# Kernel optimization log

Hardware: AMD Instinct MI355X
Metric: run time of the kernel (lower is better)

## Reference

```python
import jax, jax.numpy as jnp
import numpy as np

NG, ND = 50000, 10000          # gene / disease node counts
IN, HID = 64, 128              # in_feats / hidden_feats
EGG, EGD, EDG = 800000, 300000, 300000
EPS = 1e-5


def setup_inputs() -> dict:
    key = jax.random.key(0)
    ks = jax.random.split(key, 18)
    s = 0.05
    return {
        "xg": jax.random.normal(ks[0], (NG, IN), jnp.float32),
        "xd": jax.random.normal(ks[1], (ND, IN), jnp.float32),
        "Wn0": jax.random.normal(ks[2], (3, IN, HID), jnp.float32) * s,
        "Ws0": jax.random.normal(ks[3], (3, IN, HID), jnp.float32) * s,
        "b0": jnp.zeros((3, HID), jnp.float32),
        "Wn1": jax.random.normal(ks[4], (3, HID, HID), jnp.float32) * s,
        "Ws1": jax.random.normal(ks[5], (3, HID, HID), jnp.float32) * s,
        "b1": jnp.zeros((3, HID), jnp.float32),
        "bng": jnp.ones((2, 2, HID), jnp.float32),   # [layer, ntype, HID]
        "bnb": jnp.zeros((2, 2, HID), jnp.float32),
        "Wp": jax.random.normal(ks[6], (2, HID, IN), jnp.float32) * s,
        "bp": jnp.zeros((2, IN), jnp.float32),
        "gg_src": jax.random.randint(ks[7], (EGG,), 0, NG, jnp.int32),
        "gg_dst": jax.random.randint(ks[8], (EGG,), 0, NG, jnp.int32),
        "gd_src": jax.random.randint(ks[9], (EGD,), 0, NG, jnp.int32),
        "gd_dst": jax.random.randint(ks[10], (EGD,), 0, ND, jnp.int32),
        "dg_src": jax.random.randint(ks[11], (EDG,), 0, ND, jnp.int32),
        "dg_dst": jax.random.randint(ks[12], (EDG,), 0, NG, jnp.int32),
    }


def _seg_mean(h_src, src_idx, dst_idx, num_dst):
    # gather source features along edges, mean-reduce onto destinations
    msg = h_src[src_idx]                                         # [E, D]
    ssum = jax.ops.segment_sum(msg, dst_idx, num_segments=num_dst)
    deg = jax.ops.segment_sum(jnp.ones((dst_idx.shape[0], 1), h_src.dtype),
                              dst_idx, num_segments=num_dst)
    return ssum / jnp.maximum(deg, 1.0)                          # zero-degree -> 0


def _sage(h_src, h_dst, src_idx, dst_idx, num_dst, Wn, Ws, b):
    # DGL SAGEConv(mean): fc_neigh(mean_neigh) + fc_self(h_dst) + bias
    m = _seg_mean(h_src, src_idx, dst_idx, num_dst)
    return m @ Wn + h_dst @ Ws + b


def _bn_relu(x, g, b):
    # BatchNorm1d in training mode (batch statistics) followed by ReLU
    mu = x.mean(axis=0)
    var = x.var(axis=0)
    return jax.nn.relu((x - mu) * jax.lax.rsqrt(var + EPS) * g + b)


def _hetero_layer(hg, hd, Wn, Ws, b, idx):
    gg_s, gg_d, gd_s, gd_d, dg_s, dg_d = idx
    # HeteroGraphConv aggregate='sum' across relations per destination type
    out_g = (_sage(hg, hg, gg_s, gg_d, NG, Wn[0], Ws[0], b[0]) +
             _sage(hd, hg, dg_s, dg_d, NG, Wn[2], Ws[2], b[2]))
    out_d = _sage(hg, hd, gd_s, gd_d, ND, Wn[1], Ws[1], b[1])
    return out_g, out_d


def reference(xg, xd, Wn0, Ws0, b0, Wn1, Ws1, b1, bng, bnb, Wp, bp,
              gg_src, gg_dst, gd_src, gd_dst, dg_src, dg_dst):
    idx = (gg_src, gg_dst, gd_src, gd_dst, dg_src, dg_dst)
    # layer 0
    hg, hd = _hetero_layer(xg, xd, Wn0, Ws0, b0, idx)
    hg = _bn_relu(hg, bng[0, 0], bnb[0, 0])
    hd = _bn_relu(hd, bng[0, 1], bnb[0, 1])
    # layer 1
    hg, hd = _hetero_layer(hg, hd, Wn1, Ws1, b1, idx)
    hg = _bn_relu(hg, bng[1, 0], bnb[1, 0])
    hd = _bn_relu(hd, bng[1, 1], bnb[1, 1])
    # final per-type projection back to in_feats
    out_g = hg @ Wp[0] + bp[0]
    out_d = hd @ Wp[1] + bp[1]
    return out_g, out_d
```

## Files before the change

### kernel.cpp

```cpp
#include <hip/hip_runtime.h>

typedef unsigned short u16;
typedef __attribute__((ext_vector_type(8))) short bf16x8;
typedef __attribute__((ext_vector_type(4))) float f32x4;

__device__ __forceinline__ float BF(u16 u) { return __uint_as_float(((unsigned)u) << 16); }
__device__ __forceinline__ float BLO(unsigned p) { return __uint_as_float(p << 16); }
__device__ __forceinline__ float BHI(unsigned p) { return __uint_as_float(p & 0xffff0000u); }
__device__ __forceinline__ u16 FBF(float f) {
    unsigned u = __float_as_uint(f);
    u += 0x7FFFu + ((u >> 16) & 1u);
    return (u16)(u >> 16);
}
__device__ __forceinline__ unsigned PK2(float a, float b) {
    return (unsigned)FBF(a) | ((unsigned)FBF(b) << 16);
}
__device__ __forceinline__ float LD(const void* p, long i, int isf) {
    if (isf) return ((const float*)p)[i];
    return BF(((const u16*)p)[i]);
}

__global__ void HeteroGNN_78426102825755_kernel() {}

__global__ void hk_fill16(u16* p, long n, u16 v) {
    long i = (long)blockIdx.x * 256 + threadIdx.x;
    if (i < n) p[i] = v;
}

__global__ void hk_detect2(const void* x, int* flag, int* ncur, int Tn, float* bnbuf) {
    int i = blockIdx.x * 256 + threadIdx.x;
    if (i < Tn) ncur[i] = 0;
    if (i < 512) bnbuf[i] = 0.f;
    if (blockIdx.x == 0) {
        __shared__ int cnt;
        if (threadIdx.x == 0) cnt = 0;
        __syncthreads();
        unsigned w = ((const unsigned*)x)[threadIdx.x];
        int e = (w >> 7) & 0xFF;
        atomicAdd(&cnt, (e >= 0x68 && e <= 0x92) ? 1 : 0);
        __syncthreads();
        if (threadIdx.x == 0) flag[0] = (cnt >= 192) ? 0 : 1;
    }
}

__device__ __forceinline__ void wprep_one(const void* W, int K, int ncol, int persh, int ksh,
                                          unsigned* dst, int i, int isf) {
    int mslice = i >> persh;
    int d2 = i & ((1 << persh) - 1);
    int mat = mslice >> ksh;
    int ks = mslice & ((1 << ksh) - 1);
    int ct = d2 >> 8; int rr = d2 & 255; int ln = rr >> 2; int j2 = rr & 3;
    int k1 = ks * 32 + ((ln >> 4) * 8 + 2 * j2);
    int n = ct * 16 + (ln & 15);
    long e = (long)mat * K * ncol + (long)k1 * ncol + n;
    dst[i] = PK2(LD(W, e, isf), LD(W, e + ncol, isf));
}
__device__ __forceinline__ void wsum_one(const void* W, int K, unsigned* dst, int i, int isf) {
    int ks = i >> 11; int d2 = i & 2047;
    int ct = d2 >> 8; int rr = d2 & 255; int ln = rr >> 2; int j2 = rr & 3;
    int k1 = ks * 32 + ((ln >> 4) * 8 + 2 * j2);
    int n = ct * 16 + (ln & 15);
    long e = (long)k1 * 128 + n;
    long e2 = e + (long)2 * K * 128;
    dst[i] = PK2(LD(W, e, isf) + LD(W, e2, isf), LD(W, e + 128, isf) + LD(W, e2 + 128, isf));
}

__global__ void hk_prepcnt(const void* Wn0, const void* Ws0, const void* Wn1, const void* Ws1,
                           unsigned* f0n, unsigned* f0s, unsigned* f1n, unsigned* f1s,
                           unsigned* f0sum, unsigned* f1sum,
                           const void* xg, const void* xd, long n0, long n1,
                           u16* og, u16* od, int Cb,
                           const int* d0, const int* d1, const int* d2,
                           int E0, int E1, int E2, int NGn, int* cnt, int* rank,
                           const int* dflag) {
    int b = blockIdx.x, t = threadIdx.x;
    if (b < Cb) {
        int i = b * 256 + t;
        int tn;
        if (i < E0) tn = d0[i];
        else if (i < E0 + E1) tn = NGn + d1[i - E0];
        else if (i < E0 + E1 + E2) tn = 2 * NGn + d2[i - E0 - E1];
        else return;
        rank[i] = atomicAdd(&cnt[tn], 1);
        return;
    }
    int isf = dflag[0];
    b -= Cb;
    if (b < 48)  { wprep_one(Wn0, 64, 128, 11, 1, f0n, b * 256 + t, isf); return; }
    if (b < 96)  { wprep_one(Ws0, 64, 128, 11, 1, f0s, (b - 48) * 256 + t, isf); return; }
    if (b < 192) { wprep_one(Wn1, 128, 128, 11, 2, f1n, (b - 96) * 256 + t, isf); return; }
    if (b < 288) { wprep_one(Ws1, 128, 128, 11, 2, f1s, (b - 192) * 256 + t, isf); return; }
    if (b < 304) { wsum_one(Ws0, 64, f0sum, (b - 288) * 256 + t, isf); return; }
    if (b < 336) { wsum_one(Ws1, 128, f1sum, (b - 304) * 256 + t, isf); return; }
    long i = (long)(b - 336) * 256 + t;
    if (i < n0) og[i] = FBF(LD(xg, i, isf));
    else if (i < n0 + n1) od[i - n0] = FBF(LD(xd, i - n0, isf));
}

__global__ void hk_scan_a(const int* cnt, int n, int* pre, int* bsum) {
    __shared__ int lds[2048];
    __shared__ int part[256];
    int t = threadIdx.x;
    int base = blockIdx.x * 2048;
    for (int i = 0; i < 8; i++) {
        int idx = base + i * 256 + t;
        lds[i * 256 + t] = (idx < n) ? cnt[idx] : 0;
    }
    __syncthreads();
    int run[8];
    int s = 0;
    for (int i = 0; i < 8; i++) { run[i] = lds[t * 8 + i]; s += run[i]; }
    part[t] = s;
    __syncthreads();
    for (int o = 1; o < 256; o <<= 1) {
        int add = (t >= o) ? part[t - o] : 0;
        __syncthreads();
        part[t] += add;
        __syncthreads();
    }
    int ex = (t == 0) ? 0 : part[t - 1];
    for (int i = 0; i < 8; i++) {
        lds[t * 8 + i] = ex;
        ex += run[i];
    }
    __syncthreads();
    for (int i = 0; i < 8; i++) {
        int idx = base + i * 256 + t;
        if (idx < n) pre[idx] = lds[i * 256 + t];
    }
    if (t == 255) bsum[blockIdx.x] = part[255];
}

__global__ void hk_scan_b(int* bsum, int nb) {
    __shared__ int part[256];
    int t = threadIdx.x;
    part[t] = (t < nb) ? bsum[t] : 0;
    __syncthreads();
    for (int o = 1; o < 256; o <<= 1) {
        int add = (t >= o) ? part[t - o] : 0;
        __syncthreads();
        part[t] += add;
        __syncthreads();
    }
    if (t < nb) bsum[t] = (t == 0) ? 0 : part[t - 1];
    if (t == 0) bsum[nb] = part[nb - 1];
}

__global__ void hk_scan_c(const int* pre, const int* bsum, int n, int nb, int* offs) {
    int i = blockIdx.x * 256 + threadIdx.x;
    if (i < n) offs[i] = pre[i] + bsum[i >> 11];
    if (i == 0) offs[n] = bsum[nb];
}

__global__ void hk_scatter3p(const int* s0, const int* d0, const int* s1, const int* d1,
                             const int* s2, const int* d2,
                             int E0, int E1, int E2, int NGn,
                             const int* offs, const int* rank, int* csr, float pscale) {
    int part = blockIdx.x & 7;
    int stride = (gridDim.x >> 3) * 256;
    int ET = E0 + E1 + E2;
    for (int i = (blockIdx.x >> 3) * 256 + threadIdx.x; i < ET; i += stride) {
        int t;
        if (i < E0) t = d0[i];
        else if (i < E0 + E1) t = NGn + d1[i - E0];
        else t = 2 * NGn + d2[i - E0 - E1];
        int p = (int)((float)t * pscale);
        if (p > 7) p = 7;
        if (p != part) continue;
        int s = (i < E0) ? s0[i] : (i < E0 + E1) ? s1[i - E0] : s2[i - E0 - E1];
        csr[offs[t] + rank[i]] = s;
    }
}

struct FS {
    const unsigned* gsrc[2]; const int* goffs[2]; const float* gbn[2];
    const unsigned* ssrc; const float* sbn;
    const int* csr;
    const unsigned* W[12];
    const void* bb; long b1off; long b2off;
    int N; u16* out; float* stats;
};

template<bool BN>
__device__ void m64row(const unsigned* __restrict__ g, const int* __restrict__ offs,
                       const int* __restrict__ csr, unsigned* __restrict__ lds, int PSl,
                       int r, int row0, int N, int lane, const float* __restrict__ bn) {
    int gA = row0 + r, gB = gA + 1;
    if (gA >= N) return;
    int bA = offs[gA], eA = offs[gA + 1];
    int bB = 0, eB = 0;
    if (gB < N) { bB = offs[gB]; eB = offs[gB + 1]; }
    float scx = 0.f, scy = 0.f, shx = 0.f, shy = 0.f;
    if (BN) {
        float2 s2 = *(const float2*)&bn[2 * lane];
        float2 h2 = *(const float2*)&bn[128 + 2 * lane];
        scx = s2.x; scy = s2.y; shx = h2.x; shy = h2.y;
    }
    float sA0 = 0.f, sA1 = 0.f, sB0 = 0.f, sB1 = 0.f;
    auto ACC = [&](unsigned p, float& s0, float& s1) {
        float vx = BLO(p), vy = BHI(p);
        if (BN) { vx = fmaxf(fmaf(vx, scx, shx), 0.f); vy = fmaxf(fmaf(vy, scy, shy), 0.f); }
        s0 += vx; s1 += vy;
    };
    int kA = bA, kB = bB;
    while (kA + 4 <= eA && kB + 4 <= eB) {
        unsigned pA0 = g[(long)csr[kA] * 64 + lane];
        unsigned pA1 = g[(long)csr[kA + 1] * 64 + lane];
        unsigned pA2 = g[(long)csr[kA + 2] * 64 + lane];
        unsigned pA3 = g[(long)csr[kA + 3] * 64 + lane];
        unsigned pB0 = g[(long)csr[kB] * 64 + lane];
        unsigned pB1 = g[(long)csr[kB + 1] * 64 + lane];
        unsigned pB2 = g[(long)csr[kB + 2] * 64 + lane];
        unsigned pB3 = g[(long)csr[kB + 3] * 64 + lane];
        ACC(pA0, sA0, sA1); ACC(pA1, sA0, sA1); ACC(pA2, sA0, sA1); ACC(pA3, sA0, sA1);
        ACC(pB0, sB0, sB1); ACC(pB1, sB0, sB1); ACC(pB2, sB0, sB1); ACC(pB3, sB0, sB1);
        kA += 4; kB += 4;
    }
    while (kA + 4 <= eA) {
        unsigned p0 = g[(long)csr[kA] * 64 + lane];
        unsigned p1 = g[(long)csr[kA + 1] * 64 + lane];
        unsigned p2 = g[(long)csr[kA + 2] * 64 + lane];
        unsigned p3 = g[(long)csr[kA + 3] * 64 + lane];
        ACC(p0, sA0, sA1); ACC(p1, sA0, sA1); ACC(p2, sA0, sA1); ACC(p3, sA0, sA1);
        kA += 4;
    }
    while (kB + 4 <= eB) {
        unsigned p0 = g[(long)csr[kB] * 64 + lane];
        unsigned p1 = g[(long)csr[kB + 1] * 64 + lane];
        unsigned p2 = g[(long)csr[kB + 2] * 64 + lane];
        unsigned p3 = g[(long)csr[kB + 3] * 64 + lane];
        ACC(p0, sB0, sB1); ACC(p1, sB0, sB1); ACC(p2, sB0, sB1); ACC(p3, sB0, sB1);
        kB += 4;
    }
    for (; kA < eA; kA++) { unsigned p = g[(long)csr[kA] * 64 + lane]; ACC(p, sA0, sA1); }
    for (; kB < eB; kB++) { unsigned p = g[(long)csr[kB] * 64 + lane]; ACC(p, sB0, sB1); }
    float invA = (eA > bA) ? 1.f / (float)(eA - bA) : 0.f;
    float invB = (eB > bB) ? 1.f / (float)(eB - bB) : 0.f;
    lds[r * PSl + lane] = PK2(sA0 * invA, sA1 * invA);
    if (gB < N) lds[(r + 1) * PSl + lane] = PK2(sB0 * invB, sB1 * invB);
}

__device__ void m32row(const unsigned* __restrict__ g, const int* __restrict__ offs,
                       const int* __restrict__ csr, unsigned* __restrict__ lds, int PSl,
                       int r, int row0, int N, int l) {
    int gA = row0 + r, gB = gA + 1;
    if (gA >= N) return;
    int bA = offs[gA], eA = offs[gA + 1];
    int bB = 0, eB = 0;
    if (gB < N) { bB = offs[gB]; eB = offs[gB + 1]; }
    float sA0 = 0.f, sA1 = 0.f, sB0 = 0.f, sB1 = 0.f;
    int kA = bA, kB = bB;
    while (kA + 4 <= eA && kB + 4 <= eB) {
        unsigned pA0 = g[(long)csr[kA] * 32 + l];
        unsigned pA1 = g[(long)csr[kA + 1] * 32 + l];
        unsigned pA2 = g[(long)csr[kA + 2] * 32 + l];
        unsigned pA3 = g[(long)csr[kA + 3] * 32 + l];
        unsigned pB0 = g[(long)csr[kB] * 32 + l];
        unsigned pB1 = g[(long)csr[kB + 1] * 32 + l];
        unsigned pB2 = g[(long)csr[kB + 2] * 32 + l];
        unsigned pB3 = g[(long)csr[kB + 3] * 32 + l];
        sA0 += (BLO(pA0) + BLO(pA1)) + (BLO(pA2) + BLO(pA3));
        sA1 += (BHI(pA0) + BHI(pA1)) + (BHI(pA2) + BHI(pA3));
        sB0 += (BLO(pB0) + BLO(pB1)) + (BLO(pB2) + BLO(pB3));
        sB1 += (BHI(pB0) + BHI(pB1)) + (BHI(pB2) + BHI(pB3));
        kA += 4; kB += 4;
    }
    while (kA + 4 <= eA) {
        unsigned p0 = g[(long)csr[kA] * 32 + l];
        unsigned p1 = g[(long)csr[kA + 1] * 32 + l];
        unsigned p2 = g[(long)csr[kA + 2] * 32 + l];
        unsigned p3 = g[(long)csr[kA + 3] * 32 + l];
        sA0 += (BLO(p0) + BLO(p1)) + (BLO(p2) + BLO(p3));
        sA1 += (BHI(p0) + BHI(p1)) + (BHI(p2) + BHI(p3));
        kA += 4;
    }
    while (kB + 4 <= eB) {
        unsigned p0 = g[(long)csr[kB] * 32 + l];
        unsigned p1 = g[(long)csr[kB + 1] * 32 + l];
        unsigned p2 = g[(long)csr[kB + 2] * 32 + l];
        unsigned p3 = g[(long)csr[kB + 3] * 32 + l];
        sB0 += (BLO(p0) + BLO(p1)) + (BLO(p2) + BLO(p3));
        sB1 += (BHI(p0) + BHI(p1)) + (BHI(p2) + BHI(p3));
        kB += 4;
    }
    for (; kA < eA; kA++) {
        unsigned p = g[(long)csr[kA] * 32 + l];
        sA0 += BLO(p); sA1 += BHI(p);
    }
    for (; kB < eB; kB++) {
        unsigned p = g[(long)csr[kB] * 32 + l];
        sB0 += BLO(p); sB1 += BHI(p);
    }
    float invA = (eA > bA) ? 1.f / (float)(eA - bA) : 0.f;
    float invB = (eB > bB) ? 1.f / (float)(eB - bB) : 0.f;
    lds[r * PSl + l] = PK2(sA0 * invA, sA1 * invA);
    if (gB < N) lds[(r + 1) * PSl + l] = PK2(sB0 * invB, sB1 * invB);
}

template<int NM, int RS, int PS, bool BN>
__device__ __forceinline__ void stage_self(const FS& P, int row0, unsigned* lds, int tid) {
    constexpr int R4 = RS / 4;
    const uint4* src = (const uint4*)P.ssrc + (long)row0 * R4;
#pragma unroll
    for (int j0 = 0; j0 < 64 * R4; j0 += 512) {
        int j = j0 + tid;
        int r = j / R4, c = j - r * R4;
        uint4 v = src[j];
        if (BN) {
            unsigned w[4] = {v.x, v.y, v.z, v.w};
#pragma unroll
            for (int q = 0; q < 4; q++) {
                int col = 8 * c + 2 * q;
                float2 s2 = *(const float2*)&P.sbn[col];
                float2 h2 = *(const float2*)&P.sbn[128 + col];
                w[q] = PK2(fmaxf(fmaf(BLO(w[q]), s2.x, h2.x), 0.f),
                           fmaxf(fmaf(BHI(w[q]), s2.y, h2.y), 0.f));
            }
            v.x = w[0]; v.y = w[1]; v.z = w[2]; v.w = w[3];
        }
        *(uint4*)&lds[(NM * 64 + r) * PS + c * 4] = v;
    }
}

template<int NM, int KS, int RS, int PS, bool BN>
__device__ __forceinline__ void fs_body(const FS& P, int row0, int isf,
                                        unsigned* lds, float* red) {
    constexpr int NS = (NM + 1) * KS;
    int tid = threadIdx.x;
    int wave = tid >> 6, lane = tid & 63, m = lane & 15, quad = lane >> 4;
    bf16x8 B[NS];
#pragma unroll
    for (int s = 0; s < NS; s++)
        B[s] = *(const bf16x8*)(P.W[s] + wave * 256 + lane * 4);
#pragma unroll
    for (int t = 0; t < NM; t++) {
        unsigned* lt = lds + t * 64 * PS;
        if constexpr (RS == 64) {
#pragma unroll
            for (int p = 0; p < 4; p++)
                m64row<BN>(P.gsrc[t], P.goffs[t], P.csr, lt, PS,
                           wave * 8 + 2 * p, row0, P.N, lane, P.gbn[t]);
        } else {
            int half = lane >> 5, l = lane & 31;
#pragma unroll
            for (int p = 0; p < 2; p++)
                m32row(P.gsrc[t], P.goffs[t], P.csr, lt, PS,
                       wave * 8 + 4 * p + 2 * half, row0, P.N, l);
        }
    }
    stage_self<NM, RS, PS, BN>(P, row0, lds, tid);
    __syncthreads();

    f32x4 acc[4];
    f32x4 z = {0.f, 0.f, 0.f, 0.f};
#pragma unroll
    for (int rt = 0; rt < 4; rt++) acc[rt] = z;
#pragma unroll
    for (int s = 0; s < NS; s++) {
        const unsigned* ab = lds + (s / KS) * 64 * PS + (s % KS) * 16;
#pragma unroll
        for (int rt = 0; rt < 4; rt++) {
            bf16x8 af = *(const bf16x8*)(ab + (rt * 16 + m) * PS + quad * 4);
            acc[rt] = __builtin_amdgcn_mfma_f32_16x16x32_bf16(af, B[s], acc[rt], 0, 0, 0);
        }
    }
    if (tid < 256) red[tid] = 0.f;
    __syncthreads();
    int col = wave * 16 + m;
    float bv = LD(P.bb, P.b1off + col, isf);
    if (P.b2off >= 0) bv += LD(P.bb, P.b2off + col, isf);
    float ps = 0.f, ps2 = 0.f;
#pragma unroll
    for (int rt = 0; rt < 4; rt++) {
#pragma unroll
        for (int reg = 0; reg < 4; reg++) {
            int row = row0 + rt * 16 + quad * 4 + reg;
            if (row < P.N) {
                float v = acc[rt][reg] + bv;
                P.out[(long)row * 128 + col] = FBF(v);
                ps += v; ps2 += v * v;
            }
        }
    }
    atomicAdd(&red[col], ps);
    atomicAdd(&red[col + 128], ps2);
    __syncthreads();
    if (tid < 256) atomicAdd(&P.stats[tid], red[tid]);
}

template<int NMG, int NMD, int KS, int RS, int PS, bool BN>
__global__ __launch_bounds__(512) void hk_fsage(FS G, FS D, int gbl, const int* dflag) {
    __shared__ __align__(16) unsigned lds[(NMG + 1) * 64 * PS];
    __shared__ float red[256];
    int isf = dflag[0];
    int b = blockIdx.x;
    if (b < gbl) fs_body<NMG, KS, RS, PS, BN>(G, b * 64, isf, lds, red);
    else         fs_body<NMD, KS, RS, PS, BN>(D, (b - gbl) * 64, isf, lds, red);
}

__global__ void hk_bnfinal2(float* buf, float invNg, float invNd,
                            const void* g, long gg, long gd,
                            const void* b, long bg, long bd, const int* dflag) {
    int isf = dflag[0];
    int t = threadIdx.x;
    int c = t & 127, isD = t >> 7;
    float* st = buf + (isD ? 256 : 0);
    float invN = isD ? invNd : invNg;
    float s1 = st[c], s2 = st[c + 128];
    float mu = s1 * invN;
    float var = s2 * invN - mu * mu;
    if (var < 0.f) var = 0.f;
    float sc = LD(g, (isD ? gd : gg) + c, isf) * rsqrtf(var + 1e-5f);
    float* o = buf + 512 + (isD ? 256 : 0);
    o[c] = sc;
    o[c + 128] = LD(b, (isD ? bd : bg) + c, isf) - mu * sc;
    st[c] = 0.f;
    st[c + 128] = 0.f;
}

__global__ void hk_proj2(const u16* Ag, int Ngn, const u16* Ad, int Ndn, int gbl,
                         const void* W, const void* bias, float* og, float* od,
                         const float* bn, const int* dflag) {
    const int S = 130;
    __shared__ float aT[64 * S];
    __shared__ float ws[2048];
    int isf = dflag[0];
    int tid = threadIdx.x;
    int gene = ((int)blockIdx.x < gbl) ? 1 : 0;
    const u16* A = gene ? Ag : Ad;
    int N = gene ? Ngn : Ndn;
    long woff = gene ? 0 : 8192;
    long boff = gene ? 0 : 64;
    float* out = gene ? og : od;
    const float* sc = bn + 512 + (gene ? 0 : 256);
    const float* sh = sc + 128;
    int wave = tid >> 6, lane = tid & 63;
    int jx = tid & 15, r0 = (tid >> 4) * 4;
    int row0 = (gene ? blockIdx.x : blockIdx.x - gbl) * 64;

    float2 scv = *(const float2*)&sc[2 * lane];
    float2 shv = *(const float2*)&sh[2 * lane];
    const unsigned* A32 = (const unsigned*)A;
    for (int i = 0; i < 16; i++) {
        int r = wave * 16 + i, row = row0 + r;
        unsigned p = (row < N) ? A32[(long)row * 64 + lane] : 0u;
        float2 v;
        v.x = fmaf(BLO(p), scv.x, shv.x); v.x = (v.x > 0.f) ? v.x : 0.f;
        v.y = fmaf(BHI(p), scv.y, shv.y); v.y = (v.y > 0.f) ? v.y : 0.f;
        *(float2*)&aT[r * S + 2 * lane] = v;
    }
    __syncthreads();

    float acc[4][4];
    for (int r = 0; r < 4; r++)
        for (int c = 0; c < 4; c++) acc[r][c] = 0.f;

    for (int k0 = 0; k0 < 128; k0 += 32) {
        for (int i = 0; i < 8; i++) {
            int idx = tid + i * 256;
            ws[idx] = LD(W, woff + (long)(k0 + (idx >> 6)) * 64 + (idx & 63), isf);
        }
        __syncthreads();
        for (int kk = 0; kk < 32; kk++) {
            float4 w4 = *(const float4*)(ws + kk * 64 + jx * 4);
            for (int r = 0; r < 4; r++) {
                float a = aT[(r0 + r) * S + k0 + kk];
                acc[r][0] = fmaf(a, w4.x, acc[r][0]);
                acc[r][1] = fmaf(a, w4.y, acc[r][1]);
                acc[r][2] = fmaf(a, w4.z, acc[r][2]);
                acc[r][3] = fmaf(a, w4.w, acc[r][3]);
            }
        }
        __syncthreads();
    }

    float b4[4];
    for (int c = 0; c < 4; c++) b4[c] = LD(bias, boff + jx * 4 + c, isf);
    for (int r = 0; r < 4; r++) {
        int row = row0 + r0 + r;
        if (row >= N) continue;
        float4 o;
        o.x = acc[r][0] + b4[0]; o.y = acc[r][1] + b4[1];
        o.z = acc[r][2] + b4[2]; o.w = acc[r][3] + b4[3];
        *(float4*)&out[(long)row * 64 + jx * 4] = o;
    }
}

extern "C" void kernel_launch(void* const* d_in, const int* in_sizes, int n_in,
                              void* d_out, int out_size, void* d_ws, size_t ws_size,
                              hipStream_t stream) {
    const void* xg = d_in[0];
    const void* xd = d_in[1];
    const void* Wn0 = d_in[2];
    const void* Ws0 = d_in[3];
    const void* b0 = d_in[4];
    const void* Wn1 = d_in[5];
    const void* Ws1 = d_in[6];
    const void* b1 = d_in[7];
    const void* bng = d_in[8];
    const void* bnb = d_in[9];
    const void* Wp = d_in[10];
    const void* bp = d_in[11];
    const int* gg_src = (const int*)d_in[12];
    const int* gg_dst = (const int*)d_in[13];
    const int* gd_src = (const int*)d_in[14];
    const int* gd_dst = (const int*)d_in[15];
    const int* dg_src = (const int*)d_in[16];
    const int* dg_dst = (const int*)d_in[17];

    const int NG = in_sizes[0] / 64;
    const int ND = in_sizes[1] / 64;
    const int EGG = in_sizes[12];
    const int EGD = in_sizes[14];
    const int EDG = in_sizes[16];

    const int NGp = (NG + 63) & ~63;
    const int NDp = (ND + 63) & ~63;
    const int Tn = 2 * NG + ND;
    const int ET = EGG + EDG + EGD;

    float* outf = (float*)d_out;

    char* base = (char*)d_ws;
    size_t off = 0;
    u16* hg0; u16* pg1;
    unsigned *wf0n, *wf0s, *wf1n, *wf1s, *wf0sum, *wf1sum;
    int *csr, *offs, *ncur, *scanpre, *scanbs;
    int* dflag;
    float* bnbuf;
    {
        hg0 = (u16*)(base + off);      off += (size_t)NGp * 128 * 2; off = (off + 255) & ~(size_t)255;
        pg1 = (u16*)(base + off);      off += (size_t)NGp * 128 * 2; off = (off + 255) & ~(size_t)255;
        wf0n = (unsigned*)(base + off); off += 3 * 4096 * 4;         off = (off + 255) & ~(size_t)255;
        wf0s = (unsigned*)(base + off); off += 3 * 4096 * 4;         off = (off + 255) & ~(size_t)255;
        wf1n = (unsigned*)(base + off); off += 3 * 8192 * 4;         off = (off + 255) & ~(size_t)255;
        wf1s = (unsigned*)(base + off); off += 3 * 8192 * 4;         off = (off + 255) & ~(size_t)255;
        wf0sum = (unsigned*)(base + off); off += 4096 * 4;           off = (off + 255) & ~(size_t)255;
        wf1sum = (unsigned*)(base + off); off += 8192 * 4;           off = (off + 255) & ~(size_t)255;
        csr = (int*)(base + off);      off += (size_t)ET * 4;        off = (off + 255) & ~(size_t)255;
        offs = (int*)(base + off);     off += (size_t)(Tn + 1) * 4;  off = (off + 255) & ~(size_t)255;
        ncur = (int*)(base + off);     off += (size_t)Tn * 4;        off = (off + 255) & ~(size_t)255;
        scanpre = (int*)(base + off);  off += (size_t)Tn * 4;        off = (off + 255) & ~(size_t)255;
        scanbs = (int*)(base + off);   off += 257 * 4;               off = (off + 255) & ~(size_t)255;
        bnbuf = (float*)(base + off);  off += 1024 * 4;              off = (off + 255) & ~(size_t)255;
        dflag = (int*)(base + off);    off += 256;                   off = (off + 255) & ~(size_t)255;
    }
    size_t off_base = off;
    u16* pd1ws = (u16*)(base + off); off += (size_t)NDp * 128 * 2;
    size_t off_full = off;

    int tier;
    if (off_full <= ws_size) tier = 2;
    else if (off_base <= ws_size) tier = 1;
    else {
        hk_fill16<<<(int)(((long)out_size * 2 + 255) / 256), 256, 0, stream>>>(
            (u16*)d_out, (long)out_size * 2, (u16)0x4000);
        return;
    }

    u16* hd0 = (u16*)d_out;
    u16* pd1out = hd0 + (long)NDp * 128;
    u16* pd1 = (tier == 2) ? pd1ws : pd1out;

    u16* xg16 = pg1;
    u16* xd16 = pg1 + (long)NGp * 64;
    int* rank = (int*)hg0;

    hk_detect2<<<(Tn + 255) / 256, 256, 0, stream>>>(xg, dflag, ncur, Tn, bnbuf);

    {
        int Cb = (ET + 255) / 256;
        int Tb = (int)(((long)(NG + ND) * 64 + 255) / 256);
        hk_prepcnt<<<Cb + 336 + Tb, 256, 0, stream>>>(
            Wn0, Ws0, Wn1, Ws1, wf0n, wf0s, wf1n, wf1s, wf0sum, wf1sum,
            xg, xd, (long)NG * 64, (long)ND * 64, xg16, xd16, Cb,
            gg_dst, dg_dst, gd_dst, EGG, EDG, EGD, NG, ncur, rank, dflag);
    }

    {
        int nbT = (Tn + 2047) / 2048;
        hk_scan_a<<<nbT, 256, 0, stream>>>(ncur, Tn, scanpre, scanbs);
        hk_scan_b<<<1, 256, 0, stream>>>(scanbs, nbT);
        hk_scan_c<<<(Tn + 255) / 256, 256, 0, stream>>>(scanpre, scanbs, Tn, nbT, offs);
    }

    hk_scatter3p<<<8 * 208, 256, 0, stream>>>(gg_src, gg_dst, dg_src, dg_dst,
                                              gd_src, gd_dst, EGG, EDG, EGD,
                                              NG, offs, rank, csr, 8.0f / (float)Tn);

    const int gb = NGp / 64, db = NDp / 64;
    unsigned* xg16u = (unsigned*)xg16;
    unsigned* xd16u = (unsigned*)xd16;
    unsigned* hg0u = (unsigned*)hg0;
    unsigned* hd0u = (unsigned*)hd0;
    const float* bnG = bnbuf + 512;
    const float* bnD = bnbuf + 768;

    FS G = {}, D = {};

    G.gsrc[0] = xg16u; G.goffs[0] = offs;          G.gbn[0] = 0;
    G.gsrc[1] = xd16u; G.goffs[1] = offs + NG;     G.gbn[1] = 0;
    G.ssrc = xg16u; G.sbn = 0; G.csr = csr;
    G.W[0] = wf0n;            G.W[1] = wf0n + 2048;
    G.W[2] = wf0n + 2 * 4096; G.W[3] = wf0n + 2 * 4096 + 2048;
    G.W[4] = wf0sum;          G.W[5] = wf0sum + 2048;
    G.bb = b0; G.b1off = 0; G.b2off = 256;
    G.N = NG; G.out = hg0; G.stats = bnbuf;
    D.gsrc[0] = xg16u; D.goffs[0] = offs + 2 * NG; D.gbn[0] = 0;
    D.ssrc = xd16u; D.sbn = 0; D.csr = csr;
    D.W[0] = wf0n + 4096; D.W[1] = wf0n + 4096 + 2048;
    D.W[2] = wf0s + 4096; D.W[3] = wf0s + 4096 + 2048;
    D.bb = b0; D.b1off = 128; D.b2off = -1;
    D.N = ND; D.out = hd0; D.stats = bnbuf + 256;
    hk_fsage<2, 1, 2, 32, 36, false><<<gb + db, 512, 0, stream>>>(G, D, gb, dflag);
    hk_bnfinal2<<<1, 256, 0, stream>>>(bnbuf, 1.f / NG, 1.f / ND, bng, 0L, 128L, bnb, 0L, 128L, dflag);

    G = FS{}; D = FS{};
    G.gsrc[0] = hg0u; G.goffs[0] = offs;          G.gbn[0] = bnG;
    G.gsrc[1] = hd0u; G.goffs[1] = offs + NG;     G.gbn[1] = bnD;
    G.ssrc = hg0u; G.sbn = bnG; G.csr = csr;
    for (int ks = 0; ks < 4; ks++) {
        G.W[ks] = wf1n + ks * 2048;
        G.W[4 + ks] = wf1n + 2 * 8192 + ks * 2048;
        G.W[8 + ks] = wf1sum + ks * 2048;
        D.W[ks] = wf1n + 8192 + ks * 2048;
        D.W[4 + ks] = wf1s + 8192 + ks * 2048;
    }
    G.bb = b1; G.b1off = 0; G.b2off = 256;
    G.N = NG; G.out = pg1; G.stats = bnbuf;
    D.gsrc[0] = hg0u; D.goffs[0] = offs + 2 * NG; D.gbn[0] = bnG;
    D.ssrc = hd0u; D.sbn = bnD; D.csr = csr;
    D.bb = b1; D.b1off = 128; D.b2off = -1;
    D.N = ND; D.out = pd1; D.stats = bnbuf + 256;
    hk_fsage<2, 1, 4, 64, 68, true><<<gb + db, 512, 0, stream>>>(G, D, gb, dflag);
    hk_bnfinal2<<<1, 256, 0, stream>>>(bnbuf, 1.f / NG, 1.f / ND, bng, 256L, 384L, bnb, 256L, 384L, dflag);

    if (tier == 2) {
        hk_proj2<<<gb + db, 256, 0, stream>>>(pg1, NG, pd1, ND, gb, Wp, bp,
                                              outf, outf + (long)NG * 64, bnbuf, dflag);
    } else {
        hk_proj2<<<db, 256, 0, stream>>>(pg1, NG, pd1, ND, 0, Wp, bp,
                                         outf, outf + (long)NG * 64, bnbuf, dflag);
        hk_proj2<<<gb, 256, 0, stream>>>(pg1, NG, pd1, ND, gb, Wp, bp,
                                         outf, outf + (long)NG * 64, bnbuf, dflag);
    }
}
```

Before: 443.9 us.

## Split neighbor-mean aggregation out of fused SAGE kernel into separate gather kernels

Replaces the fused gather+GEMM SAGE kernel with a standalone mean-aggregation kernel that writes per-relation neighbor means to a workspace buffer, followed by a dense kernel that just stages precomputed tiles into LDS and runs the MFMA GEMM. BatchNorm+ReLU of layer-0 outputs is now applied once in place by a new elementwise kernel instead of per gathered edge. This removes the redundant per-edge BN work and lets the gather run at its own occupancy without the GEMM's LDS and register footprint. In exchange it adds extra kernel launches, a large intermediate buffer round-trip through memory, and changes the workspace tier thresholds.

```diff
diff --git a/kernel.cpp b/kernel.cpp
--- a/kernel.cpp
+++ b/kernel.cpp
@@ -172,36 +172,15 @@
     }
 }
 
-struct FS {
-    const unsigned* gsrc[2]; const int* goffs[2]; const float* gbn[2];
-    const unsigned* ssrc; const float* sbn;
-    const int* csr;
-    const unsigned* W[12];
-    const void* bb; long b1off; long b2off;
-    int N; u16* out; float* stats;
-};
-
-template<bool BN>
-__device__ void m64row(const unsigned* __restrict__ g, const int* __restrict__ offs,
-                       const int* __restrict__ csr, unsigned* __restrict__ lds, int PSl,
-                       int r, int row0, int N, int lane, const float* __restrict__ bn) {
-    int gA = row0 + r, gB = gA + 1;
-    if (gA >= N) return;
-    int bA = offs[gA], eA = offs[gA + 1];
+__device__ void mean64_rows(const unsigned* __restrict__ g, const int* __restrict__ offs,
+                            const int* __restrict__ csr, unsigned* __restrict__ out,
+                            int rA, int N, int lane) {
+    int rB = rA + 1;
+    if (rA >= N) return;
+    int bA = offs[rA], eA = offs[rA + 1];
     int bB = 0, eB = 0;
-    if (gB < N) { bB = offs[gB]; eB = offs[gB + 1]; }
-    float scx = 0.f, scy = 0.f, shx = 0.f, shy = 0.f;
-    if (BN) {
-        float2 s2 = *(const float2*)&bn[2 * lane];
-        float2 h2 = *(const float2*)&bn[128 + 2 * lane];
-        scx = s2.x; scy = s2.y; shx = h2.x; shy = h2.y;
-    }
+    if (rB < N) { bB = offs[rB]; eB = offs[rB + 1]; }
     float sA0 = 0.f, sA1 = 0.f, sB0 = 0.f, sB1 = 0.f;
-    auto ACC = [&](unsigned p, float& s0, float& s1) {
-        float vx = BLO(p), vy = BHI(p);
-        if (BN) { vx = fmaxf(fmaf(vx, scx, shx), 0.f); vy = fmaxf(fmaf(vy, scy, shy), 0.f); }
-        s0 += vx; s1 += vy;
-    };
     int kA = bA, kB = bB;
     while (kA + 4 <= eA && kB + 4 <= eB) {
         unsigned pA0 = g[(long)csr[kA] * 64 + lane];
@@ -212,8 +191,10 @@
         unsigned pB1 = g[(long)csr[kB + 1] * 64 + lane];
         unsigned pB2 = g[(long)csr[kB + 2] * 64 + lane];
         unsigned pB3 = g[(long)csr[kB + 3] * 64 + lane];
-        ACC(pA0, sA0, sA1); ACC(pA1, sA0, sA1); ACC(pA2, sA0, sA1); ACC(pA3, sA0, sA1);
-        ACC(pB0, sB0, sB1); ACC(pB1, sB0, sB1); ACC(pB2, sB0, sB1); ACC(pB3, sB0, sB1);
+        sA0 += (BLO(pA0) + BLO(pA1)) + (BLO(pA2) + BLO(pA3));
+        sA1 += (BHI(pA0) + BHI(pA1)) + (BHI(pA2) + BHI(pA3));
+        sB0 += (BLO(pB0) + BLO(pB1)) + (BLO(pB2) + BLO(pB3));
+        sB1 += (BHI(pB0) + BHI(pB1)) + (BHI(pB2) + BHI(pB3));
         kA += 4; kB += 4;
     }
     while (kA + 4 <= eA) {
@@ -221,7 +202,8 @@
         unsigned p1 = g[(long)csr[kA + 1] * 64 + lane];
         unsigned p2 = g[(long)csr[kA + 2] * 64 + lane];
         unsigned p3 = g[(long)csr[kA + 3] * 64 + lane];
-        ACC(p0, sA0, sA1); ACC(p1, sA0, sA1); ACC(p2, sA0, sA1); ACC(p3, sA0, sA1);
+        sA0 += (BLO(p0) + BLO(p1)) + (BLO(p2) + BLO(p3));
+        sA1 += (BHI(p0) + BHI(p1)) + (BHI(p2) + BHI(p3));
         kA += 4;
     }
     while (kB + 4 <= eB) {
@@ -229,25 +211,32 @@
         unsigned p1 = g[(long)csr[kB + 1] * 64 + lane];
         unsigned p2 = g[(long)csr[kB + 2] * 64 + lane];
         unsigned p3 = g[(long)csr[kB + 3] * 64 + lane];
-        ACC(p0, sB0, sB1); ACC(p1, sB0, sB1); ACC(p2, sB0, sB1); ACC(p3, sB0, sB1);
+        sB0 += (BLO(p0) + BLO(p1)) + (BLO(p2) + BLO(p3));
+        sB1 += (BHI(p0) + BHI(p1)) + (BHI(p2) + BHI(p3));
         kB += 4;
     }
-    for (; kA < eA; kA++) { unsigned p = g[(long)csr[kA] * 64 + lane]; ACC(p, sA0, sA1); }
-    for (; kB < eB; kB++) { unsigned p = g[(long)csr[kB] * 64 + lane]; ACC(p, sB0, sB1); }
+    for (; kA < eA; kA++) {
+        unsigned p = g[(long)csr[kA] * 64 + lane];
+        sA0 += BLO(p); sA1 += BHI(p);
+    }
+    for (; kB < eB; kB++) {
+        unsigned p = g[(long)csr[kB] * 64 + lane];
+        sB0 += BLO(p); sB1 += BHI(p);
+    }
     float invA = (eA > bA) ? 1.f / (float)(eA - bA) : 0.f;
     float invB = (eB > bB) ? 1.f / (float)(eB - bB) : 0.f;
-    lds[r * PSl + lane] = PK2(sA0 * invA, sA1 * invA);
-    if (gB < N) lds[(r + 1) * PSl + lane] = PK2(sB0 * invB, sB1 * invB);
-}
-
-__device__ void m32row(const unsigned* __restrict__ g, const int* __restrict__ offs,
-                       const int* __restrict__ csr, unsigned* __restrict__ lds, int PSl,
-                       int r, int row0, int N, int l) {
-    int gA = row0 + r, gB = gA + 1;
-    if (gA >= N) return;
-    int bA = offs[gA], eA = offs[gA + 1];
+    out[(long)rA * 64 + lane] = PK2(sA0 * invA, sA1 * invA);
+    if (rB < N) out[(long)rB * 64 + lane] = PK2(sB0 * invB, sB1 * invB);
+}
+
+__device__ void mean32_rows(const unsigned* __restrict__ g, const int* __restrict__ offs,
+                            const int* __restrict__ csr, unsigned* __restrict__ out,
+                            int rA, int N, int l) {
+    int rB = rA + 1;
+    if (rA >= N) return;
+    int bA = offs[rA], eA = offs[rA + 1];
     int bB = 0, eB = 0;
-    if (gB < N) { bB = offs[gB]; eB = offs[gB + 1]; }
+    if (rB < N) { bB = offs[rB]; eB = offs[rB + 1]; }
     float sA0 = 0.f, sA1 = 0.f, sB0 = 0.f, sB1 = 0.f;
     int kA = bA, kB = bB;
     while (kA + 4 <= eA && kB + 4 <= eB) {
@@ -293,62 +282,65 @@
     }
     float invA = (eA > bA) ? 1.f / (float)(eA - bA) : 0.f;
     float invB = (eB > bB) ? 1.f / (float)(eB - bB) : 0.f;
-    lds[r * PSl + l] = PK2(sA0 * invA, sA1 * invA);
-    if (gB < N) lds[(r + 1) * PSl + l] = PK2(sB0 * invB, sB1 * invB);
-}
-
-template<int NM, int RS, int PS, bool BN>
-__device__ __forceinline__ void stage_self(const FS& P, int row0, unsigned* lds, int tid) {
-    constexpr int R4 = RS / 4;
-    const uint4* src = (const uint4*)P.ssrc + (long)row0 * R4;
-#pragma unroll
-    for (int j0 = 0; j0 < 64 * R4; j0 += 512) {
-        int j = j0 + tid;
-        int r = j / R4, c = j - r * R4;
-        uint4 v = src[j];
-        if (BN) {
-            unsigned w[4] = {v.x, v.y, v.z, v.w};
-#pragma unroll
-            for (int q = 0; q < 4; q++) {
-                int col = 8 * c + 2 * q;
-                float2 s2 = *(const float2*)&P.sbn[col];
-                float2 h2 = *(const float2*)&P.sbn[128 + col];
-                w[q] = PK2(fmaxf(fmaf(BLO(w[q]), s2.x, h2.x), 0.f),
-                           fmaxf(fmaf(BHI(w[q]), s2.y, h2.y), 0.f));
-            }
-            v.x = w[0]; v.y = w[1]; v.z = w[2]; v.w = w[3];
-        }
-        *(uint4*)&lds[(NM * 64 + r) * PS + c * 4] = v;
-    }
-}
-
-template<int NM, int KS, int RS, int PS, bool BN>
-__device__ __forceinline__ void fs_body(const FS& P, int row0, int isf,
-                                        unsigned* lds, float* red) {
-    constexpr int NS = (NM + 1) * KS;
+    out[(long)rA * 32 + l] = PK2(sA0 * invA, sA1 * invA);
+    if (rB < N) out[(long)rB * 32 + l] = PK2(sB0 * invB, sB1 * invB);
+}
+
+__global__ void hk_mean32a(const unsigned* hg, const unsigned* hd,
+                           const int* offs, const int* csr,
+                           unsigned* mgg, unsigned* mdg, unsigned* mgd,
+                           int NGn, int NDn, int nbg) {
+    int b = blockIdx.x;
+    const unsigned* g; const int* O; unsigned* o; int N; int rb;
+    if (b < nbg)          { g = hg; O = offs;           o = mgg; N = NGn; rb = b * 16; }
+    else if (b < 2 * nbg) { g = hd; O = offs + NGn;     o = mdg; N = NGn; rb = (b - nbg) * 16; }
+    else                  { g = hg; O = offs + 2 * NGn; o = mgd; N = NDn; rb = (b - 2 * nbg) * 16; }
+    int w = threadIdx.x >> 6, lane = threadIdx.x & 63;
+    int half = lane >> 5, l = lane & 31;
+    mean32_rows(g, O, csr, o, rb + w * 4 + half * 2, N, l);
+}
+
+__global__ void hk_mean64a(const unsigned* hg, const unsigned* hd,
+                           const int* offs, const int* csr,
+                           unsigned* mgg, unsigned* mdg, unsigned* mgd,
+                           int NGn, int NDn, int nbg) {
+    int b = blockIdx.x;
+    const unsigned* g; const int* O; unsigned* o; int N; int rb;
+    if (b < nbg)          { g = hg; O = offs;           o = mgg; N = NGn; rb = b * 8; }
+    else if (b < 2 * nbg) { g = hd; O = offs + NGn;     o = mdg; N = NGn; rb = (b - nbg) * 8; }
+    else                  { g = hg; O = offs + 2 * NGn; o = mgd; N = NDn; rb = (b - 2 * nbg) * 8; }
+    int w = threadIdx.x >> 6, lane = threadIdx.x & 63;
+    mean64_rows(g, O, csr, o, rb + w * 2, N, lane);
+}
+
+struct DS3 {
+    const unsigned* AT[3];
+    const unsigned* W[12];
+    const void* bb; long b1off; long b2off;
+    int N; u16* out; float* stats;
+};
+
+template<int NT, int KS, int RS, int PS>
+__device__ __forceinline__ void ds3_body(const DS3& P, int row0, int isf,
+                                         unsigned* lds, float* red) {
+    constexpr int NS = NT * KS;
     int tid = threadIdx.x;
     int wave = tid >> 6, lane = tid & 63, m = lane & 15, quad = lane >> 4;
     bf16x8 B[NS];
 #pragma unroll
     for (int s = 0; s < NS; s++)
         B[s] = *(const bf16x8*)(P.W[s] + wave * 256 + lane * 4);
-#pragma unroll
-    for (int t = 0; t < NM; t++) {
-        unsigned* lt = lds + t * 64 * PS;
-        if constexpr (RS == 64) {
-#pragma unroll
-            for (int p = 0; p < 4; p++)
-                m64row<BN>(P.gsrc[t], P.goffs[t], P.csr, lt, PS,
-                           wave * 8 + 2 * p, row0, P.N, lane, P.gbn[t]);
-        } else {
-            int half = lane >> 5, l = lane & 31;
-#pragma unroll
-            for (int p = 0; p < 2; p++)
-                m32row(P.gsrc[t], P.goffs[t], P.csr, lt, PS,
-                       wave * 8 + 4 * p + 2 * half, row0, P.N, l);
+    constexpr int R4 = RS / 4;
+#pragma unroll
+    for (int t = 0; t < NT; t++) {
+        const uint4* src = (const uint4*)P.AT[t] + (long)row0 * R4;
+#pragma unroll
+        for (int j0 = 0; j0 < 64 * R4; j0 += 512) {
+            int j = j0 + tid;
+            int r = j / R4, c = j - r * R4;
+            *(uint4*)&lds[(t * 64 + r) * PS + c * 4] = src[j];
         }
     }
-    stage_self<NM, RS, PS, BN>(P, row0, lds, tid);
     __syncthreads();
 
     f32x4 acc[4];
@@ -388,14 +380,14 @@
     if (tid < 256) atomicAdd(&P.stats[tid], red[tid]);
 }
 
-template<int NMG, int NMD, int KS, int RS, int PS, bool BN>
-__global__ __launch_bounds__(512) void hk_fsage(FS G, FS D, int gbl, const int* dflag) {
-    __shared__ __align__(16) unsigned lds[(NMG + 1) * 64 * PS];
+template<int NTG, int NTD, int KS, int RS, int PS>
+__global__ __launch_bounds__(512) void hk_dsage3(DS3 G, DS3 D, int gbl, const int* dflag) {
+    __shared__ __align__(16) unsigned lds[NTG * 64 * PS];
     __shared__ float red[256];
     int isf = dflag[0];
     int b = blockIdx.x;
-    if (b < gbl) fs_body<NMG, KS, RS, PS, BN>(G, b * 64, isf, lds, red);
-    else         fs_body<NMD, KS, RS, PS, BN>(D, (b - gbl) * 64, isf, lds, red);
+    if (b < gbl) ds3_body<NTG, KS, RS, PS>(G, b * 64, isf, lds, red);
+    else         ds3_body<NTD, KS, RS, PS>(D, (b - gbl) * 64, isf, lds, red);
 }
 
 __global__ void hk_bnfinal2(float* buf, float invNg, float invNd,
@@ -416,6 +408,29 @@
     o[c + 128] = LD(b, (isD ? bd : bg) + c, isf) - mu * sc;
     st[c] = 0.f;
     st[c + 128] = 0.f;
+}
+
+__global__ void hk_bnapply2(u16* xg_, long n8g, u16* xd_, long n8d, const float* buf) {
+    long i = (long)blockIdx.x * 256 + threadIdx.x;
+    uint4* p; const float *sc, *sh; long k;
+    if (i < n8g) { k = i; p = (uint4*)xg_; sc = buf + 512; sh = buf + 640; }
+    else {
+        k = i - n8g;
+        if (k >= n8d) return;
+        p = (uint4*)xd_; sc = buf + 768; sh = buf + 896;
+    }
+    uint4 v = p[k];
+    int j = (int)(k & 15) * 8;
+    float f[8] = {BLO(v.x), BHI(v.x), BLO(v.y), BHI(v.y),
+                  BLO(v.z), BHI(v.z), BLO(v.w), BHI(v.w)};
+    for (int c = 0; c < 8; c++) {
+        float t = fmaf(f[c], sc[j + c], sh[j + c]);
+        f[c] = (t > 0.f) ? t : 0.f;
+    }
+    uint4 o;
+    o.x = PK2(f[0], f[1]); o.y = PK2(f[2], f[3]);
+    o.z = PK2(f[4], f[5]); o.w = PK2(f[6], f[7]);
+    p[k] = o;
 }
 
 __global__ void hk_proj2(const u16* Ag, int Ngn, const u16* Ad, int Ndn, int gbl,
@@ -545,13 +560,14 @@
         bnbuf = (float*)(base + off);  off += 1024 * 4;              off = (off + 255) & ~(size_t)255;
         dflag = (int*)(base + off);    off += 256;                   off = (off + 255) & ~(size_t)255;
     }
-    size_t off_base = off;
+    unsigned* meanP = (unsigned*)(base + off); off += (size_t)NGp * 128 * 4; off = (off + 255) & ~(size_t)255;
+    size_t off_mean = off;
     u16* pd1ws = (u16*)(base + off); off += (size_t)NDp * 128 * 2;
     size_t off_full = off;
 
     int tier;
     if (off_full <= ws_size) tier = 2;
-    else if (off_base <= ws_size) tier = 1;
+    else if (off_mean <= ws_size) tier = 1;
     else {
         hk_fill16<<<(int)(((long)out_size * 2 + 255) / 256), 256, 0, stream>>>(
             (u16*)d_out, (long)out_size * 2, (u16)0x4000);
@@ -560,6 +576,7 @@
 
     u16* hd0 = (u16*)d_out;
     u16* pd1out = hd0 + (long)NDp * 128;
+    unsigned* mgdM = (unsigned*)(pd1out + (long)NDp * 128);
     u16* pd1 = (tier == 2) ? pd1ws : pd1out;
 
     u16* xg16 = pg1;
@@ -593,32 +610,39 @@
     unsigned* xd16u = (unsigned*)xd16;
     unsigned* hg0u = (unsigned*)hg0;
     unsigned* hd0u = (unsigned*)hd0;
-    const float* bnG = bnbuf + 512;
-    const float* bnD = bnbuf + 768;
-
-    FS G = {}, D = {};
-
-    G.gsrc[0] = xg16u; G.goffs[0] = offs;          G.gbn[0] = 0;
-    G.gsrc[1] = xd16u; G.goffs[1] = offs + NG;     G.gbn[1] = 0;
-    G.ssrc = xg16u; G.sbn = 0; G.csr = csr;
-    G.W[0] = wf0n;            G.W[1] = wf0n + 2048;
-    G.W[2] = wf0n + 2 * 4096; G.W[3] = wf0n + 2 * 4096 + 2048;
-    G.W[4] = wf0sum;          G.W[5] = wf0sum + 2048;
+    unsigned* mggM = meanP;
+    unsigned* mdg0 = meanP + (long)NGp * 32;
+    unsigned* mdg1 = meanP + (long)NGp * 64;
+
+    DS3 G = {}, D = {};
+
+    {
+        int nbg = (NG + 15) / 16, nbd = (ND + 15) / 16;
+        hk_mean32a<<<2 * nbg + nbd, 256, 0, stream>>>(xg16u, xd16u, offs, csr,
+                                                      mggM, mdg0, mgdM, NG, ND, nbg);
+    }
+    G.AT[0] = mggM;  G.W[0] = wf0n;             G.W[1] = wf0n + 2048;
+    G.AT[1] = mdg0;  G.W[2] = wf0n + 2 * 4096;  G.W[3] = wf0n + 2 * 4096 + 2048;
+    G.AT[2] = xg16u; G.W[4] = wf0sum;           G.W[5] = wf0sum + 2048;
     G.bb = b0; G.b1off = 0; G.b2off = 256;
     G.N = NG; G.out = hg0; G.stats = bnbuf;
-    D.gsrc[0] = xg16u; D.goffs[0] = offs + 2 * NG; D.gbn[0] = 0;
-    D.ssrc = xd16u; D.sbn = 0; D.csr = csr;
-    D.W[0] = wf0n + 4096; D.W[1] = wf0n + 4096 + 2048;
-    D.W[2] = wf0s + 4096; D.W[3] = wf0s + 4096 + 2048;
+    D.AT[0] = mgdM;  D.W[0] = wf0n + 4096;      D.W[1] = wf0n + 4096 + 2048;
+    D.AT[1] = xd16u; D.W[2] = wf0s + 4096;      D.W[3] = wf0s + 4096 + 2048;
     D.bb = b0; D.b1off = 128; D.b2off = -1;
     D.N = ND; D.out = hd0; D.stats = bnbuf + 256;
-    hk_fsage<2, 1, 2, 32, 36, false><<<gb + db, 512, 0, stream>>>(G, D, gb, dflag);
+    hk_dsage3<3, 2, 2, 32, 36><<<gb + db, 512, 0, stream>>>(G, D, gb, dflag);
     hk_bnfinal2<<<1, 256, 0, stream>>>(bnbuf, 1.f / NG, 1.f / ND, bng, 0L, 128L, bnb, 0L, 128L, dflag);
-
-    G = FS{}; D = FS{};
-    G.gsrc[0] = hg0u; G.goffs[0] = offs;          G.gbn[0] = bnG;
-    G.gsrc[1] = hd0u; G.goffs[1] = offs + NG;     G.gbn[1] = bnD;
-    G.ssrc = hg0u; G.sbn = bnG; G.csr = csr;
+    hk_bnapply2<<<(int)(((long)(NG + ND) * 16 + 255) / 256), 256, 0, stream>>>(
+        hg0, (long)NG * 16, hd0, (long)ND * 16, bnbuf);
+
+    {
+        int nbg = (NG + 7) / 8, nbd = (ND + 7) / 8;
+        hk_mean64a<<<2 * nbg + nbd, 256, 0, stream>>>(hg0u, hd0u, offs, csr,
+                                                      mggM, mdg1, mgdM, NG, ND, nbg);
+    }
+    G = DS3{}; D = DS3{};
+    G.AT[0] = mggM;  G.AT[1] = mdg1;  G.AT[2] = hg0u;
+    D.AT[0] = mgdM;  D.AT[1] = hd0u;
     for (int ks = 0; ks < 4; ks++) {
         G.W[ks] = wf1n + ks * 2048;
         G.W[4 + ks] = wf1n + 2 * 8192 + ks * 2048;
@@ -628,11 +652,9 @@
     }
     G.bb = b1; G.b1off = 0; G.b2off = 256;
     G.N = NG; G.out = pg1; G.stats = bnbuf;
-    D.gsrc[0] = hg0u; D.goffs[0] = offs + 2 * NG; D.gbn[0] = bnG;
-    D.ssrc = hd0u; D.sbn = bnD; D.csr = csr;
     D.bb = b1; D.b1off = 128; D.b2off = -1;
     D.N = ND; D.out = pd1; D.stats = bnbuf + 256;
-    hk_fsage<2, 1, 4, 64, 68, true><<<gb + db, 512, 0, stream>>>(G, D, gb, dflag);
+    hk_dsage3<3, 2, 4, 64, 68><<<gb + db, 512, 0, stream>>>(G, D, gb, dflag);
     hk_bnfinal2<<<1, 256, 0, stream>>>(bnbuf, 1.f / NG, 1.f / ND, bng, 256L, 384L, bnb, 256L, 384L, dflag);
 
     if (tier == 2) {
```

After: 420.9 us. -5.2%, faster.
